# Kernel tuning notes

Measured on AMD Instinct MI355X. Metric: run time of the kernel, lower is better.

## Reference

```python
import jax, jax.numpy as jnp
import numpy as np
from jax import lax


def _median_blur(img, k):
    # img: [B, H, W]; k odd (3 here). Replicate border like cv2.medianBlur.
    p = k // 2
    B, H, W = img.shape
    xp = jnp.pad(img, ((0, 0), (p, p), (p, p)), mode='edge')
    # Gather the k*k shifted views -> [B, H, W, k*k]
    wins = jnp.stack([xp[:, i:i + H, j:j + W] for i in range(k) for j in range(k)], axis=-1)
    return jnp.median(wins, axis=-1)


def setup_inputs() -> dict:
    key = jax.random.key(0)
    kx, kt = jax.random.split(key)
    x = jax.random.normal(kx, (32, 1, 512, 512), dtype=jnp.float32)
    t_tensor = jax.random.randint(kt, (32,), 0, 10).astype(jnp.int64)
    return {"x": x, "t_tensor": t_tensor, "kernel_size": 3, "num_timesteps": 10}


def reference(x, t_tensor, kernel_size, num_timesteps):
    # Faithful vectorized version of MedianBlur.forward_process:
    # sample i gets t_tensor[i] successive median blurs.
    B, C, H, W = x.shape  # C == 1, matching the .squeeze() in the original
    img = x[:, 0, :, :]  # [B, H, W]
    t = t_tensor.astype(jnp.int32)

    def step(cur, j):
        blurred = _median_blur(cur, kernel_size)
        active = (j < t)[:, None, None]  # only samples with t_i > j keep blurring
        return jnp.where(active, blurred, cur), None

    out, _ = lax.scan(step, img, jnp.arange(num_timesteps, dtype=jnp.int32))
    return out[:, None, :, :]  # restore channel dim, like unsqueeze(0) per sample
```

## Files before the change

### kernel.cpp

```cpp
#include <hip/hip_runtime.h>


#define TD 82
#define OW 64
#define RAD 9
#define NT 256

__device__ __forceinline__ float min3f(float a, float b, float c) { return fminf(fminf(a, b), c); }
__device__ __forceinline__ float max3f(float a, float b, float c) { return fmaxf(fmaxf(a, b), c); }
__device__ __forceinline__ float med3f(float a, float b, float c) { return __builtin_amdgcn_fmed3f(a, b, c); }

__global__ __launch_bounds__(NT) void median_fused_kernel(
    const float* __restrict__ src, float* __restrict__ dst,
    const int* __restrict__ t)
{
    __shared__ float buf[TD * TD];

    const int b   = blockIdx.y;
    const int y0  = (blockIdx.x >> 3) * OW;
    const int x0  = (blockIdx.x & 7) * OW;
    const int tid = threadIdx.x;
    const float* img  = src + (b << 18);
    float*       outb = dst + (b << 18);

    int T = t[b];
    T = min(max(T, 0), 9);

    const int sr = tid >> 4;
    const int sc = (tid & 15) << 2;

    if (T == 0) {
        #pragma unroll
        for (int rr = 0; rr < 4; ++rr) {
            int gy = y0 + sr + rr * 16;
            *(float4*)&outb[(gy << 9) + x0 + sc] =
                *(const float4*)&img[(gy << 9) + x0 + sc];
        }
        return;
    }

    for (int i = tid; i < TD * TD; i += NT) {
        int r = i / TD, c = i - r * TD;
        int gy = min(max(y0 - RAD + r, 0), 511);
        int gx = min(max(x0 - RAD + c, 0), 511);
        buf[i] = img[(gy << 9) + gx];
    }

    const bool topE = (y0 == 0), botE = (y0 == 512 - OW);
    const bool lftE = (x0 == 0), rgtE = (x0 == 512 - OW);

    const int ptx = tid & 15;
    const int pty = tid >> 4;
    const int ub  = 1 + 5 * pty;
    const int vb  = 1 + 5 * ptx;

    const bool padTop = topE && (pty == 1);
    const bool padBot = botE && (pty == 14);
    const bool padLft = lftE && (ptx == 1);
    const bool padRgt = rgtE && (ptx == 14);

    __syncthreads();

    float stage[25];
    #pragma unroll
    for (int i = 0; i < 5; ++i)
        #pragma unroll
        for (int j = 0; j < 5; ++j)
            stage[i * 5 + j] = buf[(ub + i) * TD + vb + j];

    for (int k = 0; k < T; ++k) {
        float A[7], Br[7], C[7], ns[25];
        {
            const float* p = &buf[(ub - 1) * TD + (vb - 1)];
            #pragma unroll
            for (int j = 0; j < 7; ++j) A[j] = p[j];
        }
        Br[0] = buf[ub * TD + (vb - 1)];
        #pragma unroll
        for (int j = 0; j < 5; ++j) Br[1 + j] = stage[j];
        Br[6] = buf[ub * TD + (vb + 5)];

        #pragma unroll
        for (int i = 0; i < 5; ++i) {
            if (i < 4) {
                C[0] = buf[(ub + 1 + i) * TD + (vb - 1)];
                #pragma unroll
                for (int j = 0; j < 5; ++j) C[1 + j] = stage[(i + 1) * 5 + j];
                C[6] = buf[(ub + 1 + i) * TD + (vb + 5)];
            } else {
                const float* p = &buf[(ub + 5) * TD + (vb - 1)];
                #pragma unroll
                for (int j = 0; j < 7; ++j) C[j] = p[j];
            }
            float lo[7], mi[7], hi[7];
            #pragma unroll
            for (int j = 0; j < 7; ++j) {
                lo[j] = min3f(A[j], Br[j], C[j]);
                mi[j] = med3f(A[j], Br[j], C[j]);
                hi[j] = max3f(A[j], Br[j], C[j]);
            }
            #pragma unroll
            for (int j = 0; j < 5; ++j)
                ns[i * 5 + j] = med3f(max3f(lo[j], lo[j+1], lo[j+2]),
                                      med3f(mi[j], mi[j+1], mi[j+2]),
                                      min3f(hi[j], hi[j+1], hi[j+2]));
            #pragma unroll
            for (int j = 0; j < 7; ++j) { A[j] = Br[j]; Br[j] = C[j]; }
        }

        if (padTop) {
            #pragma unroll
            for (int j = 0; j < 5; ++j) ns[10 + j] = ns[15 + j];
        }
        if (padBot) {
            #pragma unroll
            for (int j = 0; j < 5; ++j) ns[10 + j] = ns[5 + j];
        }
        if (padLft) {
            #pragma unroll
            for (int i = 0; i < 5; ++i) ns[i * 5 + 2] = ns[i * 5 + 3];
        }
        if (padRgt) {
            #pragma unroll
            for (int i = 0; i < 5; ++i) ns[i * 5 + 2] = ns[i * 5 + 1];
        }

        __syncthreads();

        if (k == T - 1) {
            #pragma unroll
            for (int i = 0; i < 5; ++i)
                #pragma unroll
                for (int j = 0; j < 5; ++j)
                    buf[(ub + i) * TD + vb + j] = ns[i * 5 + j];
        } else {
            #pragma unroll
            for (int j = 0; j < 5; ++j) buf[ub * TD + vb + j]       = ns[j];
            #pragma unroll
            for (int j = 0; j < 5; ++j) buf[(ub + 4) * TD + vb + j] = ns[20 + j];
            #pragma unroll
            for (int i = 1; i < 4; ++i) {
                buf[(ub + i) * TD + vb]     = ns[i * 5];
                buf[(ub + i) * TD + vb + 4] = ns[i * 5 + 4];
            }
        }

        #pragma unroll
        for (int m = 0; m < 25; ++m) stage[m] = ns[m];

        __syncthreads();
    }

    #pragma unroll
    for (int rr = 0; rr < 4; ++rr) {
        int row = sr + rr * 16;
        const float* s = &buf[(row + RAD) * TD + RAD + sc];
        float4 v = { s[0], s[1], s[2], s[3] };
        *(float4*)&outb[((y0 + row) << 9) + x0 + sc] = v;
    }
}

extern "C" void kernel_launch(void* const* d_in, const int* in_sizes, int n_in,
                              void* d_out, int out_size, void* d_ws, size_t ws_size,
                              hipStream_t stream) {
    const float* x   = (const float*)d_in[0];
    const int*   t   = (const int*)d_in[1];
    float*       out = (float*)d_out;

    dim3 block(NT);
    dim3 grid(64, 32);
    median_fused_kernel<<<grid, block, 0, stream>>>(x, out, t);
}
```

Measured before the change: 104.5 us.

## Shrink tiles to 32x32 with 64-thread blocks and 6x6 per-thread register patches

Reduces the output tile from 64x64 to 32x32 with a 50x50 halo tile (row stride 52) and one wavefront per block, so each thread keeps a 6x6 patch in registers instead of 5x5. The grid quadruples, giving more blocks to balance uneven per-sample blur counts across CUs. The per-step stage copy is replaced by ping-pong register arrays. In exchange, the halo overhead per output pixel rises (50²/32² versus 82²/64²) and register pressure grows.

```diff
diff --git a/kernel.cpp b/kernel.cpp
--- a/kernel.cpp
+++ b/kernel.cpp
@@ -1,24 +1,25 @@
 #include <hip/hip_runtime.h>
 
 
-#define TD 82
-#define OW 64
+#define SROW 52
+#define TROW 50
+#define OW 32
 #define RAD 9
-#define NT 256
+#define NT 64
 
 __device__ __forceinline__ float min3f(float a, float b, float c) { return fminf(fminf(a, b), c); }
 __device__ __forceinline__ float max3f(float a, float b, float c) { return fmaxf(fmaxf(a, b), c); }
 __device__ __forceinline__ float med3f(float a, float b, float c) { return __builtin_amdgcn_fmed3f(a, b, c); }
 
-__global__ __launch_bounds__(NT) void median_fused_kernel(
+__global__ __launch_bounds__(NT, 3) void median_fused_kernel(
     const float* __restrict__ src, float* __restrict__ dst,
     const int* __restrict__ t)
 {
-    __shared__ float buf[TD * TD];
+    __shared__ float buf[TROW * SROW];
 
     const int b   = blockIdx.y;
-    const int y0  = (blockIdx.x >> 3) * OW;
-    const int x0  = (blockIdx.x & 7) * OW;
+    const int y0  = (blockIdx.x >> 4) * OW;
+    const int x0  = (blockIdx.x & 15) * OW;
     const int tid = threadIdx.x;
     const float* img  = src + (b << 18);
     float*       outb = dst + (b << 18);
@@ -26,21 +27,22 @@
     int T = t[b];
     T = min(max(T, 0), 9);
 
-    const int sr = tid >> 4;
-    const int sc = (tid & 15) << 2;
+    const int rg = tid >> 3;
+    const int c4 = (tid & 7) << 2;
 
     if (T == 0) {
         #pragma unroll
-        for (int rr = 0; rr < 4; ++rr) {
-            int gy = y0 + sr + rr * 16;
-            *(float4*)&outb[(gy << 9) + x0 + sc] =
-                *(const float4*)&img[(gy << 9) + x0 + sc];
+        for (int pass = 0; pass < 4; ++pass) {
+            int gy = y0 + rg + pass * 8;
+            *(float4*)&outb[(gy << 9) + x0 + c4] =
+                *(const float4*)&img[(gy << 9) + x0 + c4];
         }
         return;
     }
 
-    for (int i = tid; i < TD * TD; i += NT) {
-        int r = i / TD, c = i - r * TD;
+    for (int i = tid; i < TROW * SROW; i += NT) {
+        int r = i / SROW, c = i - r * SROW;
+        c = min(c, TROW - 1);
         int gy = min(max(y0 - RAD + r, 0), 511);
         int gx = min(max(x0 - RAD + c, 0), 511);
         buf[i] = img[(gy << 9) + gx];
@@ -49,114 +51,122 @@
     const bool topE = (y0 == 0), botE = (y0 == 512 - OW);
     const bool lftE = (x0 == 0), rgtE = (x0 == 512 - OW);
 
-    const int ptx = tid & 15;
-    const int pty = tid >> 4;
-    const int ub  = 1 + 5 * pty;
-    const int vb  = 1 + 5 * ptx;
+    const int pty = tid >> 3;
+    const int ptx = tid & 7;
+    const int ub  = 1 + 6 * pty;
+    const int vb  = 1 + 6 * ptx;
 
     const bool padTop = topE && (pty == 1);
-    const bool padBot = botE && (pty == 14);
+    const bool padBot = botE && (pty == 6);
     const bool padLft = lftE && (ptx == 1);
-    const bool padRgt = rgtE && (ptx == 14);
+    const bool padRgt = rgtE && (ptx == 6);
+
+    auto body = [&](const float (&cur)[36], float (&nxt)[36]) {
+        float A[8], Bx[8], C[8];
+        {
+            const float* p = &buf[(ub - 1) * SROW + (vb - 1)];
+            #pragma unroll
+            for (int j = 0; j < 8; ++j) A[j] = p[j];
+        }
+        Bx[0] = buf[ub * SROW + (vb - 1)];
+        #pragma unroll
+        for (int j = 0; j < 6; ++j) Bx[1 + j] = cur[j];
+        Bx[7] = buf[ub * SROW + (vb + 6)];
+
+        #pragma unroll
+        for (int i = 0; i < 6; ++i) {
+            if (i < 5) {
+                C[0] = buf[(ub + 1 + i) * SROW + (vb - 1)];
+                #pragma unroll
+                for (int j = 0; j < 6; ++j) C[1 + j] = cur[(i + 1) * 6 + j];
+                C[7] = buf[(ub + 1 + i) * SROW + (vb + 6)];
+            } else {
+                const float* q = &buf[(ub + 6) * SROW + (vb - 1)];
+                #pragma unroll
+                for (int j = 0; j < 8; ++j) C[j] = q[j];
+            }
+            float lo[8], mi[8], hi[8];
+            #pragma unroll
+            for (int j = 0; j < 8; ++j) {
+                lo[j] = min3f(A[j], Bx[j], C[j]);
+                mi[j] = med3f(A[j], Bx[j], C[j]);
+                hi[j] = max3f(A[j], Bx[j], C[j]);
+            }
+            #pragma unroll
+            for (int j = 0; j < 6; ++j)
+                nxt[i * 6 + j] = med3f(max3f(lo[j], lo[j+1], lo[j+2]),
+                                       med3f(mi[j], mi[j+1], mi[j+2]),
+                                       min3f(hi[j], hi[j+1], hi[j+2]));
+            #pragma unroll
+            for (int j = 0; j < 8; ++j) { A[j] = Bx[j]; Bx[j] = C[j]; }
+        }
+        if (padTop) {
+            #pragma unroll
+            for (int j = 0; j < 6; ++j) nxt[6 + j]  = nxt[12 + j];
+        }
+        if (padBot) {
+            #pragma unroll
+            for (int j = 0; j < 6; ++j) nxt[24 + j] = nxt[18 + j];
+        }
+        if (padLft) {
+            #pragma unroll
+            for (int i = 0; i < 6; ++i) nxt[i * 6 + 1] = nxt[i * 6 + 2];
+        }
+        if (padRgt) {
+            #pragma unroll
+            for (int i = 0; i < 6; ++i) nxt[i * 6 + 4] = nxt[i * 6 + 3];
+        }
+    };
+
+    auto writeback = [&](const float (&ns)[36], bool full) {
+        if (full) {
+            #pragma unroll
+            for (int i = 0; i < 6; ++i)
+                #pragma unroll
+                for (int j = 0; j < 6; ++j)
+                    buf[(ub + i) * SROW + vb + j] = ns[i * 6 + j];
+        } else {
+            #pragma unroll
+            for (int j = 0; j < 6; ++j) buf[ub * SROW + vb + j]       = ns[j];
+            #pragma unroll
+            for (int j = 0; j < 6; ++j) buf[(ub + 5) * SROW + vb + j] = ns[30 + j];
+            #pragma unroll
+            for (int i = 1; i < 5; ++i) {
+                buf[(ub + i) * SROW + vb]     = ns[i * 6];
+                buf[(ub + i) * SROW + vb + 5] = ns[i * 6 + 5];
+            }
+        }
+    };
 
     __syncthreads();
 
-    float stage[25];
+    float s0[36], s1[36];
     #pragma unroll
-    for (int i = 0; i < 5; ++i)
+    for (int i = 0; i < 6; ++i)
         #pragma unroll
-        for (int j = 0; j < 5; ++j)
-            stage[i * 5 + j] = buf[(ub + i) * TD + vb + j];
+        for (int j = 0; j < 6; ++j)
+            s0[i * 6 + j] = buf[(ub + i) * SROW + vb + j];
 
     for (int k = 0; k < T; ++k) {
-        float A[7], Br[7], C[7], ns[25];
-        {
-            const float* p = &buf[(ub - 1) * TD + (vb - 1)];
-            #pragma unroll
-            for (int j = 0; j < 7; ++j) A[j] = p[j];
+        const bool last = (k == T - 1);
+        if (k & 1) {
+            body(s1, s0);
+            __syncthreads();
+            writeback(s0, last);
+        } else {
+            body(s0, s1);
+            __syncthreads();
+            writeback(s1, last);
         }
-        Br[0] = buf[ub * TD + (vb - 1)];
-        #pragma unroll
-        for (int j = 0; j < 5; ++j) Br[1 + j] = stage[j];
-        Br[6] = buf[ub * TD + (vb + 5)];
-
-        #pragma unroll
-        for (int i = 0; i < 5; ++i) {
-            if (i < 4) {
-                C[0] = buf[(ub + 1 + i) * TD + (vb - 1)];
-                #pragma unroll
-                for (int j = 0; j < 5; ++j) C[1 + j] = stage[(i + 1) * 5 + j];
-                C[6] = buf[(ub + 1 + i) * TD + (vb + 5)];
-            } else {
-                const float* p = &buf[(ub + 5) * TD + (vb - 1)];
-                #pragma unroll
-                for (int j = 0; j < 7; ++j) C[j] = p[j];
-            }
-            float lo[7], mi[7], hi[7];
-            #pragma unroll
-            for (int j = 0; j < 7; ++j) {
-                lo[j] = min3f(A[j], Br[j], C[j]);
-                mi[j] = med3f(A[j], Br[j], C[j]);
-                hi[j] = max3f(A[j], Br[j], C[j]);
-            }
-            #pragma unroll
-            for (int j = 0; j < 5; ++j)
-                ns[i * 5 + j] = med3f(max3f(lo[j], lo[j+1], lo[j+2]),
-                                      med3f(mi[j], mi[j+1], mi[j+2]),
-                                      min3f(hi[j], hi[j+1], hi[j+2]));
-            #pragma unroll
-            for (int j = 0; j < 7; ++j) { A[j] = Br[j]; Br[j] = C[j]; }
-        }
-
-        if (padTop) {
-            #pragma unroll
-            for (int j = 0; j < 5; ++j) ns[10 + j] = ns[15 + j];
-        }
-        if (padBot) {
-            #pragma unroll
-            for (int j = 0; j < 5; ++j) ns[10 + j] = ns[5 + j];
-        }
-        if (padLft) {
-            #pragma unroll
-            for (int i = 0; i < 5; ++i) ns[i * 5 + 2] = ns[i * 5 + 3];
-        }
-        if (padRgt) {
-            #pragma unroll
-            for (int i = 0; i < 5; ++i) ns[i * 5 + 2] = ns[i * 5 + 1];
-        }
-
-        __syncthreads();
-
-        if (k == T - 1) {
-            #pragma unroll
-            for (int i = 0; i < 5; ++i)
-                #pragma unroll
-                for (int j = 0; j < 5; ++j)
-                    buf[(ub + i) * TD + vb + j] = ns[i * 5 + j];
-        } else {
-            #pragma unroll
-            for (int j = 0; j < 5; ++j) buf[ub * TD + vb + j]       = ns[j];
-            #pragma unroll
-            for (int j = 0; j < 5; ++j) buf[(ub + 4) * TD + vb + j] = ns[20 + j];
-            #pragma unroll
-            for (int i = 1; i < 4; ++i) {
-                buf[(ub + i) * TD + vb]     = ns[i * 5];
-                buf[(ub + i) * TD + vb + 4] = ns[i * 5 + 4];
-            }
-        }
-
-        #pragma unroll
-        for (int m = 0; m < 25; ++m) stage[m] = ns[m];
-
         __syncthreads();
     }
 
     #pragma unroll
-    for (int rr = 0; rr < 4; ++rr) {
-        int row = sr + rr * 16;
-        const float* s = &buf[(row + RAD) * TD + RAD + sc];
+    for (int pass = 0; pass < 4; ++pass) {
+        int row = rg + pass * 8;
+        const float* s = &buf[(row + RAD) * SROW + RAD + c4];
         float4 v = { s[0], s[1], s[2], s[3] };
-        *(float4*)&outb[((y0 + row) << 9) + x0 + sc] = v;
+        *(float4*)&outb[((y0 + row) << 9) + x0 + c4] = v;
     }
 }
 
@@ -168,6 +178,6 @@
     float*       out = (float*)d_out;
 
     dim3 block(NT);
-    dim3 grid(64, 32);
+    dim3 grid(256, 32);
     median_fused_kernel<<<grid, block, 0, stream>>>(x, out, t);
 }
```

After: 131.9 us. 1.26x slower.
